# Optimization experiments

Hardware: AMD Instinct MI355X
Metric: run time of the kernel (lower is better)

## Reference

```python
import jax, jax.numpy as jnp
import numpy as np

B, S, H = 4, 2048, 2048          # batch, seq_len, hidden_size
NH, NKV, D = 8, 1, 256           # query heads, kv heads (MQA), head_dim
ROPE_THETA = 10000.0
SCALE = D ** -0.5


def setup_inputs() -> dict:
    key = jax.random.key(0)
    k1, k2, k3 = jax.random.split(key, 3)
    hidden_states = jax.random.normal(k1, (B, S, H), dtype=jnp.float32)
    w_qkv = jax.random.normal(k2, (H, (NH + 2 * NKV) * D), dtype=jnp.float32) * 0.02
    w_o = jax.random.normal(k3, (NH * D, H), dtype=jnp.float32) * 0.02
    positions = jnp.arange(S, dtype=jnp.int32)
    return {"hidden_states": hidden_states, "positions": positions,
            "w_qkv": w_qkv, "w_o": w_o}


def _apply_rope(x, positions):
    # x: [B, S, n_heads, D], neox style: rotate halves
    d2 = D // 2
    inv_freq = 1.0 / (ROPE_THETA ** (jnp.arange(0, d2, dtype=jnp.float32) * 2.0 / D))
    ang = positions.astype(jnp.float32)[:, None] * inv_freq[None, :]      # [S, d2]
    cos = jnp.cos(ang)[None, :, None, :]                                  # [1,S,1,d2]
    sin = jnp.sin(ang)[None, :, None, :]
    x1, x2 = x[..., :d2], x[..., d2:]
    return jnp.concatenate([x1 * cos - x2 * sin, x2 * cos + x1 * sin], axis=-1)


def reference(hidden_states, positions, w_qkv, w_o):
    # fused QKV projection
    qkv = jnp.einsum('bsh,hd->bsd', hidden_states, w_qkv)                 # [B,S,(NH+2NKV)*D]
    q_size, kv_size = NH * D, NKV * D
    q = qkv[..., :q_size].reshape(B, S, NH, D)
    k = qkv[..., q_size:q_size + kv_size].reshape(B, S, NKV, D)
    v = qkv[..., q_size + kv_size:].reshape(B, S, NKV, D)

    q = _apply_rope(q, positions)
    k = _apply_rope(k, positions)

    # expand KV heads for MQA/GQA
    rep = NH // NKV
    k = jnp.repeat(k, rep, axis=2)                                        # [B,S,NH,D]
    v = jnp.repeat(v, rep, axis=2)

    scores = jnp.einsum('bqhd,bkhd->bhqk', q, k) * SCALE                  # [B,NH,S,S]
    causal = jnp.tril(jnp.ones((S, S), dtype=bool))
    scores = jnp.where(causal[None, None], scores, jnp.finfo(scores.dtype).min)
    probs = jax.nn.softmax(scores, axis=-1)
    attn = jnp.einsum('bhqk,bkhd->bqhd', probs, v).reshape(B, S, NH * D)

    return jnp.einsum('bsd,dh->bsh', attn, w_o)                           # [B,S,H]
```

## Files before the change

### kernel.cpp

```cpp
#include <hip/hip_runtime.h>
#include <math.h>

constexpr int BATCH = 4;
constexpr int SEQ   = 2048;
constexpr int HID   = 2048;
constexpr int NHEAD = 8;
constexpr int HD    = 256;
constexpr int QKVN  = (NHEAD + 2) * HD;
constexpr float SCL = 0.0625f;

typedef __bf16 bf16_t;
typedef __bf16 bf16x8 __attribute__((ext_vector_type(8)));
typedef float  f32x4  __attribute__((ext_vector_type(4)));

__device__ __forceinline__ f32x4 zero4() {
  f32x4 z; z[0] = 0.f; z[1] = 0.f; z[2] = 0.f; z[3] = 0.f; return z;
}

__device__ __forceinline__ f32x4 mfma16(bf16x8 a, bf16x8 b, f32x4 c) {
  return __builtin_amdgcn_mfma_f32_16x16x32_bf16(a, b, c, 0, 0, 0);
}

__device__ __forceinline__ void gl2lds16(const void* g, void* lds) {
  typedef __attribute__((address_space(1))) void* gp_t;
  typedef __attribute__((address_space(3))) void* lp_t;
  __builtin_amdgcn_global_load_lds((gp_t)(size_t)g,
                                   (lp_t)(unsigned int)(size_t)lds, 16, 0, 0);
}

__device__ __forceinline__ float rmax16(float v) {
#pragma unroll
  for (int o = 1; o < 16; o <<= 1) v = fmaxf(v, __shfl_xor(v, o));
  return v;
}
__device__ __forceinline__ float rsum16(float v) {
#pragma unroll
  for (int o = 1; o < 16; o <<= 1) v += __shfl_xor(v, o);
  return v;
}

__global__ __launch_bounds__(256)
void cvt_bf16_kernel(const float* __restrict__ in, bf16_t* __restrict__ out) {
  const int i = blockIdx.x * 256 + threadIdx.x;
  const float4 a = ((const float4*)in)[i * 2];
  const float4 b = ((const float4*)in)[i * 2 + 1];
  bf16x8 o;
  o[0] = (bf16_t)a.x; o[1] = (bf16_t)a.y; o[2] = (bf16_t)a.z; o[3] = (bf16_t)a.w;
  o[4] = (bf16_t)b.x; o[5] = (bf16_t)b.y; o[6] = (bf16_t)b.z; o[7] = (bf16_t)b.w;
  ((bf16x8*)out)[i] = o;
}

__global__ __launch_bounds__(256)
void transw_kernel(const float* __restrict__ w, bf16_t* __restrict__ wT, int K, int N) {
  __shared__ __align__(16) bf16_t tile[64][72];
  const int n0 = blockIdx.x * 64, k0 = blockIdx.y * 64;
  const int t = threadIdx.x, rr = t >> 3, c8 = (t & 7) * 8;
#pragma unroll
  for (int it = 0; it < 2; ++it) {
    const int r = rr + it * 32;
    const float4* p = (const float4*)(w + (size_t)(k0 + r) * N + n0 + c8);
    const float4 a = p[0], b = p[1];
    bf16x8 o;
    o[0] = (bf16_t)a.x; o[1] = (bf16_t)a.y; o[2] = (bf16_t)a.z; o[3] = (bf16_t)a.w;
    o[4] = (bf16_t)b.x; o[5] = (bf16_t)b.y; o[6] = (bf16_t)b.z; o[7] = (bf16_t)b.w;
    *(bf16x8*)&tile[r][c8] = o;
  }
  __syncthreads();
#pragma unroll
  for (int it = 0; it < 2; ++it) {
    const int rn = rr + it * 32;
    bf16x8 o;
#pragma unroll
    for (int j = 0; j < 8; ++j) o[j] = tile[c8 + j][rn];
    *(bf16x8*)&wT[(size_t)(n0 + rn) * K + k0 + c8] = o;
  }
}

template <typename TC>
__global__ __launch_bounds__(256)
void gemm_bt_kernel(const bf16_t* __restrict__ A, const bf16_t* __restrict__ BT,
                    TC* __restrict__ C, int M, int N, int K) {
  __shared__ __align__(16) bf16_t As[128 * 32];
  __shared__ __align__(16) bf16_t Bs[128 * 32];
  const int tid = threadIdx.x;
  const int lane = tid & 63, w = tid >> 6;
  const int quad = lane >> 4, l15 = lane & 15;
  const int bm = blockIdx.y * 128, bn = blockIdx.x * 128;
  const int wm = (w & 1) * 64, wn = (w >> 1) * 64;
  const int r0 = tid >> 2, c0 = tid & 3;

  f32x4 acc[4][4];
#pragma unroll
  for (int mt = 0; mt < 4; ++mt)
#pragma unroll
    for (int nt = 0; nt < 4; ++nt) acc[mt][nt] = zero4();

  for (int k0 = 0; k0 < K; k0 += 32) {
#pragma unroll
    for (int i = 0; i < 2; ++i) {
      const int r = r0 + i * 64;
      const int cg = (c0 ^ (r & 3)) << 3;
      gl2lds16(A + (size_t)(bm + r) * K + k0 + cg, &As[(i * 256 + w * 64) * 8]);
      gl2lds16(BT + (size_t)(bn + r) * K + k0 + cg, &Bs[(i * 256 + w * 64) * 8]);
    }
    __syncthreads();
    bf16x8 af[4], bf[4];
#pragma unroll
    for (int mt = 0; mt < 4; ++mt) {
      const int row = wm + mt * 16 + l15;
      af[mt] = *(const bf16x8*)&As[row * 32 + ((quad ^ (row & 3)) << 3)];
    }
#pragma unroll
    for (int nt = 0; nt < 4; ++nt) {
      const int row = wn + nt * 16 + l15;
      bf[nt] = *(const bf16x8*)&Bs[row * 32 + ((quad ^ (row & 3)) << 3)];
    }
#pragma unroll
    for (int mt = 0; mt < 4; ++mt)
#pragma unroll
      for (int nt = 0; nt < 4; ++nt)
        acc[mt][nt] = mfma16(af[mt], bf[nt], acc[mt][nt]);
    __syncthreads();
  }

#pragma unroll
  for (int mt = 0; mt < 4; ++mt)
#pragma unroll
    for (int nt = 0; nt < 4; ++nt)
#pragma unroll
      for (int r = 0; r < 4; ++r) {
        const int row = bm + wm + mt * 16 + quad * 4 + r;
        const int col = bn + wn + nt * 16 + l15;
        C[(size_t)row * N + col] = (TC)acc[mt][nt][r];
      }
}

__global__ __launch_bounds__(128)
void rope_table_kernel(const int* __restrict__ pos, float2* __restrict__ tab) {
  const int s = blockIdx.x, i = threadIdx.x;
  const float inv_freq = powf(10000.0f, -(float)i / 128.0f);
  const float ang = (float)pos[s] * inv_freq;
  float sn, cs;
  sincosf(ang, &sn, &cs);
  tab[s * 128 + i] = make_float2(cs, sn);
}

__global__ __launch_bounds__(256)
void rope_kernel(const float2* __restrict__ tab, bf16_t* __restrict__ qkv) {
  const int bs = blockIdx.x * 16 + (threadIdx.x >> 4);
  const int h  = blockIdx.y;
  const int i0 = (threadIdx.x & 15) * 8;
  const int s  = bs & (SEQ - 1);
  const size_t base = (size_t)bs * QKVN + (size_t)h * HD;
  bf16x8 a = *(const bf16x8*)&qkv[base + i0];
  bf16x8 b = *(const bf16x8*)&qkv[base + 128 + i0];
  bf16x8 oa, ob;
#pragma unroll
  for (int j = 0; j < 8; ++j) {
    const float2 t = tab[s * 128 + i0 + j];
    const float x1 = (float)a[j], x2 = (float)b[j];
    oa[j] = (bf16_t)(x1 * t.x - x2 * t.y);
    ob[j] = (bf16_t)(x2 * t.x + x1 * t.y);
  }
  *(bf16x8*)&qkv[base + i0]       = oa;
  *(bf16x8*)&qkv[base + 128 + i0] = ob;
}

__global__ __launch_bounds__(256)
void vtrans_kernel(const bf16_t* __restrict__ qkv, bf16_t* __restrict__ Vt) {
  __shared__ __align__(16) bf16_t tile[64][72];
  const int s0 = blockIdx.x * 64, d0 = blockIdx.y * 64, b = blockIdx.z;
  const int t = threadIdx.x, rr = t >> 3, c8 = (t & 7) * 8;
#pragma unroll
  for (int it = 0; it < 2; ++it) {
    const int r = rr + it * 32;
    *(bf16x8*)&tile[r][c8] =
        *(const bf16x8*)&qkv[(size_t)(b * SEQ + s0 + r) * QKVN + 2304 + d0 + c8];
  }
  __syncthreads();
#pragma unroll
  for (int it = 0; it < 2; ++it) {
    const int dd = rr + it * 32;
    bf16x8 o;
#pragma unroll
    for (int j = 0; j < 8; ++j) o[j] = tile[c8 + j][dd];
    *(bf16x8*)&Vt[(size_t)(b * HD + d0 + dd) * SEQ + s0 + c8] = o;
  }
}

__global__ __launch_bounds__(512)
void attn_kernel(const bf16_t* __restrict__ qkv, const bf16_t* __restrict__ Vt,
                 bf16_t* __restrict__ O) {
  __shared__ __align__(16) bf16_t Ks[2][64 * 256];
  __shared__ __align__(16) bf16_t Vts[2][256 * 64];
  __shared__ __align__(16) bf16_t Pl[8][16][72];

  const int tid = threadIdx.x, w = tid >> 6, lane = tid & 63;
  const int quad = lane >> 4, l15 = lane & 15;
  const int b = blockIdx.x >> 6;
  const int qtR = blockIdx.x & 63;
  const int h = w;

  const int krow_base = w * 2 + (lane >> 5);
  const int kcol = lane & 31;
  const int vrow_base = w * 8 + (lane >> 3);
  const int vcol = lane & 7;

  const bf16_t* kbase0 = qkv + (size_t)(b * SEQ) * QKVN + 2048;
  const bf16_t* vbase0 = Vt + (size_t)b * HD * SEQ;

  auto stage = [&](int kt, int buf) {
    const bf16_t* kbase = kbase0 + (size_t)(kt * 64) * QKVN;
#pragma unroll
    for (int i = 0; i < 4; ++i) {
      const int r = i * 16 + krow_base;
      gl2lds16(kbase + (size_t)r * QKVN + ((kcol ^ (r & 31)) << 3),
               &Ks[buf][(i * 512 + w * 64) * 8]);
    }
    const bf16_t* vbase = vbase0 + kt * 64;
#pragma unroll
    for (int i = 0; i < 4; ++i) {
      const int r = i * 64 + vrow_base;
      gl2lds16(vbase + (size_t)r * SEQ + ((vcol ^ (r & 7)) << 3),
               &Vts[buf][(i * 512 + w * 64) * 8]);
    }
  };

  for (int phase = 0; phase < 2; ++phase) {
    const int qt = phase ? (127 - qtR) : qtR;
    const int q0 = qt * 16;

    bf16x8 qf[8];
    const bf16_t* qp =
        qkv + (size_t)(b * SEQ + q0 + l15) * QKVN + (size_t)h * HD + quad * 8;
#pragma unroll
    for (int ks = 0; ks < 8; ++ks) qf[ks] = *(const bf16x8*)(qp + ks * 32);

    float mrun[4], lrun[4];
    f32x4 of[16];
#pragma unroll
    for (int r = 0; r < 4; ++r) { mrun[r] = -3e38f; lrun[r] = 0.f; }
#pragma unroll
    for (int dt = 0; dt < 16; ++dt) of[dt] = zero4();

    const int ntiles = q0 / 64 + 1;
    int cur = 0;
    stage(0, 0);
    __syncthreads();

    for (int kt = 0; kt < ntiles; ++kt) {
      if (kt + 1 < ntiles) stage(kt + 1, cur ^ 1);

      const bf16_t* ksb = Ks[cur];
      const bf16_t* vsb = Vts[cur];

      f32x4 sf[4];
#pragma unroll
      for (int nt = 0; nt < 4; ++nt) {
        f32x4 acc = zero4();
        const int row = nt * 16 + l15;
#pragma unroll
        for (int ks = 0; ks < 8; ++ks) {
          const int j = ks * 4 + quad;
          const bf16x8 kf = *(const bf16x8*)&ksb[row * 256 + ((j ^ (row & 31)) << 3)];
          acc = mfma16(qf[ks], kf, acc);
        }
        sf[nt] = acc;
      }

      const bool lastTile = (kt == ntiles - 1);
      float mx[4];
#pragma unroll
      for (int r = 0; r < 4; ++r) {
        const int qg = q0 + quad * 4 + r;
        float v = -3e38f;
#pragma unroll
        for (int nt = 0; nt < 4; ++nt) {
          float s = sf[nt][r] * SCL;
          if (lastTile) {
            const int kg = kt * 64 + nt * 16 + l15;
            if (kg > qg) s = -3e38f;
          }
          sf[nt][r] = s;
          v = fmaxf(v, s);
        }
        mx[r] = rmax16(v);
      }

      float g = 0.f;
#pragma unroll
      for (int r = 0; r < 4; ++r) g = fmaxf(g, mx[r] - mrun[r]);
      const bool resc = !__all(g <= 8.0f);
      f32x4 av;
      if (resc) {
#pragma unroll
        for (int r = 0; r < 4; ++r) {
          const float mn = fmaxf(mrun[r], mx[r]);
          av[r] = __expf(mrun[r] - mn);
          mrun[r] = mn;
          lrun[r] *= av[r];
        }
      }

#pragma unroll
      for (int r = 0; r < 4; ++r) {
        float sum = 0.f;
#pragma unroll
        for (int nt = 0; nt < 4; ++nt) {
          const float pv = __expf(sf[nt][r] - mrun[r]);
          Pl[w][quad * 4 + r][nt * 16 + l15] = (bf16_t)pv;
          sum += pv;
        }
        lrun[r] += rsum16(sum);
      }
      if (resc) {
#pragma unroll
        for (int dt = 0; dt < 16; ++dt) of[dt] *= av;
      }
      __asm__ volatile("s_waitcnt lgkmcnt(0)" ::: "memory");

      bf16x8 pa[2];
#pragma unroll
      for (int k2 = 0; k2 < 2; ++k2)
        pa[k2] = *(const bf16x8*)&Pl[w][l15][k2 * 32 + quad * 8];
#pragma unroll
      for (int dt = 0; dt < 16; ++dt) {
        const int row = dt * 16 + l15;
#pragma unroll
        for (int k2 = 0; k2 < 2; ++k2) {
          const int j = k2 * 4 + quad;
          const bf16x8 vf = *(const bf16x8*)&vsb[row * 64 + ((j ^ (row & 7)) << 3)];
          of[dt] = mfma16(pa[k2], vf, of[dt]);
        }
      }

      __syncthreads();
      cur ^= 1;
    }

    f32x4 iv;
#pragma unroll
    for (int r = 0; r < 4; ++r) iv[r] = 1.0f / lrun[r];
#pragma unroll
    for (int dt = 0; dt < 16; ++dt) {
      const f32x4 o = of[dt] * iv;
#pragma unroll
      for (int r = 0; r < 4; ++r)
        O[(size_t)(b * SEQ + q0 + quad * 4 + r) * HID + (size_t)h * HD + dt * 16 + l15] =
            (bf16_t)o[r];
    }
  }
}

extern "C" void kernel_launch(void* const* d_in, const int* in_sizes, int n_in,
                              void* d_out, int out_size, void* d_ws, size_t ws_size,
                              hipStream_t stream) {
  const float* hidden  = (const float*)d_in[0];
  const int* positions = (const int*)d_in[1];
  const float* w_qkv   = (const float*)d_in[2];
  const float* w_o     = (const float*)d_in[3];
  float* out           = (float*)d_out;

  char* ws = (char*)d_ws;
  bf16_t* hiddenB = (bf16_t*)ws; ws += (size_t)8192 * 2048 * 2;
  bf16_t* wqkvT   = (bf16_t*)ws; ws += (size_t)2560 * 2048 * 2;
  bf16_t* woT     = (bf16_t*)ws; ws += (size_t)2048 * 2048 * 2;
  bf16_t* qkvB    = (bf16_t*)ws; ws += (size_t)8192 * 2560 * 2;
  bf16_t* VtB     = (bf16_t*)ws; ws += (size_t)4 * 256 * 2048 * 2;
  bf16_t* attnB   = (bf16_t*)ws;

  float2* ropeTab = (float2*)attnB;

  cvt_bf16_kernel<<<8192, 256, 0, stream>>>(hidden, hiddenB);
  transw_kernel<<<dim3(QKVN / 64, HID / 64), 256, 0, stream>>>(w_qkv, wqkvT, HID, QKVN);
  transw_kernel<<<dim3(HID / 64, HID / 64), 256, 0, stream>>>(w_o, woT, HID, HID);
  rope_table_kernel<<<SEQ, 128, 0, stream>>>(positions, ropeTab);

  gemm_bt_kernel<bf16_t><<<dim3(QKVN / 128, 64), 256, 0, stream>>>
      (hiddenB, wqkvT, qkvB, 8192, QKVN, HID);

  rope_kernel<<<dim3(BATCH * SEQ / 16, 9), 256, 0, stream>>>(ropeTab, qkvB);
  vtrans_kernel<<<dim3(SEQ / 64, HD / 64, BATCH), 256, 0, stream>>>(qkvB, VtB);

  attn_kernel<<<256, 512, 0, stream>>>(qkvB, VtB, attnB);

  gemm_bt_kernel<float><<<dim3(HID / 128, 64), 256, 0, stream>>>
      (attnB, woT, out, 8192, HID, HID);
}
```

Measured before the change: 510.0 us.

## Restructure attention to 32-row query tiles with 4-head blocks; swizzle GEMM block order

The attention kernel now uses 256-thread blocks of 4 heads, each wave processing two 16-row query subtiles that share every K/V fragment read from LDS. Double buffering is dropped so two blocks can fit per CU, and the P scratch buffer gets an XOR swizzle to avoid bank conflicts. The GEMM remaps block indices with an XCD-aware swizzle so neighbouring tiles land on the same L2. Without double buffering, the global loads are no longer overlapped with compute inside a block, and holding two accumulator sets raises register pressure.

```diff
diff --git a/kernel.cpp b/kernel.cpp
--- a/kernel.cpp
+++ b/kernel.cpp
@@ -85,7 +85,13 @@
   const int tid = threadIdx.x;
   const int lane = tid & 63, w = tid >> 6;
   const int quad = lane >> 4, l15 = lane & 15;
-  const int bm = blockIdx.y * 128, bn = blockIdx.x * 128;
+
+  const int nwg = gridDim.x * gridDim.y;
+  const int flat = blockIdx.y * gridDim.x + blockIdx.x;
+  const int cpx = nwg >> 3;
+  const int swz = (flat & 7) * cpx + (flat >> 3);
+  const int bm = (swz / gridDim.x) * 128, bn = (swz % gridDim.x) * 128;
+
   const int wm = (w & 1) * 64, wn = (w >> 1) * 64;
   const int r0 = tid >> 2, c0 = tid & 3;
 
@@ -188,18 +194,23 @@
   }
 }
 
-__global__ __launch_bounds__(512)
+__global__ __launch_bounds__(256, 2)
 void attn_kernel(const bf16_t* __restrict__ qkv, const bf16_t* __restrict__ Vt,
                  bf16_t* __restrict__ O) {
-  __shared__ __align__(16) bf16_t Ks[2][64 * 256];
-  __shared__ __align__(16) bf16_t Vts[2][256 * 64];
-  __shared__ __align__(16) bf16_t Pl[8][16][72];
+  __shared__ __align__(16) bf16_t Ks[64 * 256];
+  __shared__ __align__(16) bf16_t Vts[256 * 64];
+  __shared__ __align__(16) bf16_t Pl[4][32][64];
 
   const int tid = threadIdx.x, w = tid >> 6, lane = tid & 63;
   const int quad = lane >> 4, l15 = lane & 15;
-  const int b = blockIdx.x >> 6;
-  const int qtR = blockIdx.x & 63;
-  const int h = w;
+  const int bid = blockIdx.x;
+  const int j = bid & 255;
+  const int b = j >> 6;
+  const int hg = bid >> 8;
+  const int qg = hg ? (63 - (j & 63)) : (j & 63);
+  const int h = hg * 4 + w;
+  const int q0 = qg * 32;
+  const int ntiles = (q0 + 31) / 64 + 1;
 
   const int krow_base = w * 2 + (lane >> 5);
   const int kcol = lane & 31;
@@ -209,145 +220,154 @@
   const bf16_t* kbase0 = qkv + (size_t)(b * SEQ) * QKVN + 2048;
   const bf16_t* vbase0 = Vt + (size_t)b * HD * SEQ;
 
-  auto stage = [&](int kt, int buf) {
+  bf16x8 qf[2][8];
+#pragma unroll
+  for (int sub = 0; sub < 2; ++sub) {
+    const bf16_t* qp = qkv + (size_t)(b * SEQ + q0 + sub * 16 + l15) * QKVN +
+                       (size_t)h * HD + quad * 8;
+#pragma unroll
+    for (int ks = 0; ks < 8; ++ks) qf[sub][ks] = *(const bf16x8*)(qp + ks * 32);
+  }
+
+  float mrun[2][4], lrun[2][4];
+  f32x4 of[2][16];
+#pragma unroll
+  for (int sub = 0; sub < 2; ++sub) {
+#pragma unroll
+    for (int r = 0; r < 4; ++r) { mrun[sub][r] = -3e38f; lrun[sub][r] = 0.f; }
+#pragma unroll
+    for (int dt = 0; dt < 16; ++dt) of[sub][dt] = zero4();
+  }
+
+  for (int kt = 0; kt < ntiles; ++kt) {
     const bf16_t* kbase = kbase0 + (size_t)(kt * 64) * QKVN;
 #pragma unroll
-    for (int i = 0; i < 4; ++i) {
-      const int r = i * 16 + krow_base;
+    for (int i = 0; i < 8; ++i) {
+      const int r = i * 8 + krow_base;
       gl2lds16(kbase + (size_t)r * QKVN + ((kcol ^ (r & 31)) << 3),
-               &Ks[buf][(i * 512 + w * 64) * 8]);
+               &Ks[(i * 256 + w * 64) * 8]);
     }
     const bf16_t* vbase = vbase0 + kt * 64;
 #pragma unroll
-    for (int i = 0; i < 4; ++i) {
-      const int r = i * 64 + vrow_base;
+    for (int i = 0; i < 8; ++i) {
+      const int r = i * 32 + vrow_base;
       gl2lds16(vbase + (size_t)r * SEQ + ((vcol ^ (r & 7)) << 3),
-               &Vts[buf][(i * 512 + w * 64) * 8]);
-    }
-  };
-
-  for (int phase = 0; phase < 2; ++phase) {
-    const int qt = phase ? (127 - qtR) : qtR;
-    const int q0 = qt * 16;
-
-    bf16x8 qf[8];
-    const bf16_t* qp =
-        qkv + (size_t)(b * SEQ + q0 + l15) * QKVN + (size_t)h * HD + quad * 8;
-#pragma unroll
-    for (int ks = 0; ks < 8; ++ks) qf[ks] = *(const bf16x8*)(qp + ks * 32);
-
-    float mrun[4], lrun[4];
-    f32x4 of[16];
-#pragma unroll
-    for (int r = 0; r < 4; ++r) { mrun[r] = -3e38f; lrun[r] = 0.f; }
-#pragma unroll
-    for (int dt = 0; dt < 16; ++dt) of[dt] = zero4();
-
-    const int ntiles = q0 / 64 + 1;
-    int cur = 0;
-    stage(0, 0);
+               &Vts[(i * 256 + w * 64) * 8]);
+    }
     __syncthreads();
 
-    for (int kt = 0; kt < ntiles; ++kt) {
-      if (kt + 1 < ntiles) stage(kt + 1, cur ^ 1);
-
-      const bf16_t* ksb = Ks[cur];
-      const bf16_t* vsb = Vts[cur];
-
-      f32x4 sf[4];
-#pragma unroll
-      for (int nt = 0; nt < 4; ++nt) {
-        f32x4 acc = zero4();
-        const int row = nt * 16 + l15;
-#pragma unroll
-        for (int ks = 0; ks < 8; ++ks) {
-          const int j = ks * 4 + quad;
-          const bf16x8 kf = *(const bf16x8*)&ksb[row * 256 + ((j ^ (row & 31)) << 3)];
-          acc = mfma16(qf[ks], kf, acc);
-        }
-        sf[nt] = acc;
+    f32x4 sf[2][4];
+#pragma unroll
+    for (int nt = 0; nt < 4; ++nt) {
+      f32x4 a0 = zero4(), a1 = zero4();
+      const int row = nt * 16 + l15;
+#pragma unroll
+      for (int ks = 0; ks < 8; ++ks) {
+        const bf16x8 kf =
+            *(const bf16x8*)&Ks[row * 256 + (((ks * 4 + quad) ^ (row & 31)) << 3)];
+        a0 = mfma16(qf[0][ks], kf, a0);
+        a1 = mfma16(qf[1][ks], kf, a1);
       }
-
-      const bool lastTile = (kt == ntiles - 1);
-      float mx[4];
+      sf[0][nt] = a0; sf[1][nt] = a1;
+    }
+
+    const bool lastTile = (kt == ntiles - 1);
+    float mx[2][4];
+#pragma unroll
+    for (int sub = 0; sub < 2; ++sub)
 #pragma unroll
       for (int r = 0; r < 4; ++r) {
-        const int qg = q0 + quad * 4 + r;
+        const int qrow = q0 + sub * 16 + quad * 4 + r;
         float v = -3e38f;
 #pragma unroll
         for (int nt = 0; nt < 4; ++nt) {
-          float s = sf[nt][r] * SCL;
+          float s = sf[sub][nt][r] * SCL;
           if (lastTile) {
             const int kg = kt * 64 + nt * 16 + l15;
-            if (kg > qg) s = -3e38f;
+            if (kg > qrow) s = -3e38f;
           }
-          sf[nt][r] = s;
+          sf[sub][nt][r] = s;
           v = fmaxf(v, s);
         }
-        mx[r] = rmax16(v);
+        mx[sub][r] = rmax16(v);
       }
 
-      float g = 0.f;
-#pragma unroll
-      for (int r = 0; r < 4; ++r) g = fmaxf(g, mx[r] - mrun[r]);
-      const bool resc = !__all(g <= 8.0f);
-      f32x4 av;
-      if (resc) {
+    float g = 0.f;
+#pragma unroll
+    for (int sub = 0; sub < 2; ++sub)
+#pragma unroll
+      for (int r = 0; r < 4; ++r) g = fmaxf(g, mx[sub][r] - mrun[sub][r]);
+    const bool resc = !__all(g <= 8.0f);
+    f32x4 av[2];
+    if (resc) {
+#pragma unroll
+      for (int sub = 0; sub < 2; ++sub)
 #pragma unroll
         for (int r = 0; r < 4; ++r) {
-          const float mn = fmaxf(mrun[r], mx[r]);
-          av[r] = __expf(mrun[r] - mn);
-          mrun[r] = mn;
-          lrun[r] *= av[r];
+          const float mn = fmaxf(mrun[sub][r], mx[sub][r]);
+          av[sub][r] = __expf(mrun[sub][r] - mn);
+          mrun[sub][r] = mn;
+          lrun[sub][r] *= av[sub][r];
         }
-      }
-
+    }
+
+#pragma unroll
+    for (int sub = 0; sub < 2; ++sub)
 #pragma unroll
       for (int r = 0; r < 4; ++r) {
+        const int rowp = sub * 16 + quad * 4 + r;
         float sum = 0.f;
 #pragma unroll
         for (int nt = 0; nt < 4; ++nt) {
-          const float pv = __expf(sf[nt][r] - mrun[r]);
-          Pl[w][quad * 4 + r][nt * 16 + l15] = (bf16_t)pv;
+          const float pv = __expf(sf[sub][nt][r] - mrun[sub][r]);
+          Pl[w][rowp][(((nt * 2 + (l15 >> 3)) ^ (rowp & 7)) << 3) + (l15 & 7)] =
+              (bf16_t)pv;
           sum += pv;
         }
-        lrun[r] += rsum16(sum);
+        lrun[sub][r] += rsum16(sum);
       }
-      if (resc) {
-#pragma unroll
-        for (int dt = 0; dt < 16; ++dt) of[dt] *= av;
+    if (resc) {
+#pragma unroll
+      for (int sub = 0; sub < 2; ++sub)
+#pragma unroll
+        for (int dt = 0; dt < 16; ++dt) of[sub][dt] *= av[sub];
+    }
+    __asm__ volatile("s_waitcnt lgkmcnt(0)" ::: "memory");
+
+    bf16x8 pa[2][2];
+#pragma unroll
+    for (int sub = 0; sub < 2; ++sub)
+#pragma unroll
+      for (int k2 = 0; k2 < 2; ++k2)
+        pa[sub][k2] = *(const bf16x8*)
+            &Pl[w][sub * 16 + l15][(((k2 * 4 + quad) ^ (l15 & 7)) << 3)];
+#pragma unroll
+    for (int dt = 0; dt < 16; ++dt) {
+      const int row = dt * 16 + l15;
+#pragma unroll
+      for (int k2 = 0; k2 < 2; ++k2) {
+        const bf16x8 vf =
+            *(const bf16x8*)&Vts[row * 64 + (((k2 * 4 + quad) ^ (row & 7)) << 3)];
+        of[0][dt] = mfma16(pa[0][k2], vf, of[0][dt]);
+        of[1][dt] = mfma16(pa[1][k2], vf, of[1][dt]);
       }
-      __asm__ volatile("s_waitcnt lgkmcnt(0)" ::: "memory");
-
-      bf16x8 pa[2];
-#pragma unroll
-      for (int k2 = 0; k2 < 2; ++k2)
-        pa[k2] = *(const bf16x8*)&Pl[w][l15][k2 * 32 + quad * 8];
-#pragma unroll
-      for (int dt = 0; dt < 16; ++dt) {
-        const int row = dt * 16 + l15;
-#pragma unroll
-        for (int k2 = 0; k2 < 2; ++k2) {
-          const int j = k2 * 4 + quad;
-          const bf16x8 vf = *(const bf16x8*)&vsb[row * 64 + ((j ^ (row & 7)) << 3)];
-          of[dt] = mfma16(pa[k2], vf, of[dt]);
-        }
-      }
-
-      __syncthreads();
-      cur ^= 1;
-    }
-
+    }
+
+    __syncthreads();
+  }
+
+#pragma unroll
+  for (int sub = 0; sub < 2; ++sub) {
     f32x4 iv;
 #pragma unroll
-    for (int r = 0; r < 4; ++r) iv[r] = 1.0f / lrun[r];
+    for (int r = 0; r < 4; ++r) iv[r] = 1.0f / lrun[sub][r];
 #pragma unroll
     for (int dt = 0; dt < 16; ++dt) {
-      const f32x4 o = of[dt] * iv;
+      const f32x4 o = of[sub][dt] * iv;
 #pragma unroll
       for (int r = 0; r < 4; ++r)
-        O[(size_t)(b * SEQ + q0 + quad * 4 + r) * HID + (size_t)h * HD + dt * 16 + l15] =
-            (bf16_t)o[r];
+        O[(size_t)(b * SEQ + q0 + sub * 16 + quad * 4 + r) * HID +
+          (size_t)h * HD + dt * 16 + l15] = (bf16_t)o[r];
     }
   }
 }
@@ -382,7 +402,7 @@
   rope_kernel<<<dim3(BATCH * SEQ / 16, 9), 256, 0, stream>>>(ropeTab, qkvB);
   vtrans_kernel<<<dim3(SEQ / 64, HD / 64, BATCH), 256, 0, stream>>>(qkvB, VtB);
 
-  attn_kernel<<<256, 512, 0, stream>>>(qkvB, VtB, attnB);
+  attn_kernel<<<512, 256, 0, stream>>>(qkvB, VtB, attnB);
 
   gemm_bt_kernel<float><<<dim3(HID / 128, 64), 256, 0, stream>>>
       (attnB, woT, out, 8192, HID, HID);
```

After: 776.0 us. 1.52x slower.

## Replace GEMM with 256x256-tile, 512-thread double-buffered pipelined kernel

Applied to the files above, without the earlier changes.

Replaces the simple 128x128 single-buffered bf16 GEMM with a 256x256 tile kernel using 8 waves and a 64-wide K step. Global-to-LDS loads are double-buffered and interleaved with MFMA phases, using explicit waitcnt, barriers and setprio. The goal is to raise data reuse per tile and hide memory latency behind matrix math in both projection GEMMs. In exchange it needs 128KB of LDS, which limits occupancy, and launches fewer blocks (320 and 256), which risks poor CU fill on a 256-CU part.

```diff
diff --git a/kernel.cpp b/kernel.cpp
--- a/kernel.cpp
+++ b/kernel.cpp
@@ -76,63 +76,145 @@
   }
 }
 
+#define BAR()   __builtin_amdgcn_s_barrier()
+#define LGKM0() do { asm volatile("s_waitcnt lgkmcnt(0)" ::: "memory"); \
+                     __builtin_amdgcn_sched_barrier(0); } while (0)
+#define VMC(n)  asm volatile("s_waitcnt vmcnt(" #n ")" ::: "memory")
+
 template <typename TC>
-__global__ __launch_bounds__(256)
-void gemm_bt_kernel(const bf16_t* __restrict__ A, const bf16_t* __restrict__ BT,
+__global__ __launch_bounds__(512)
+void gemm256_kernel(const bf16_t* __restrict__ A, const bf16_t* __restrict__ BT,
                     TC* __restrict__ C, int M, int N, int K) {
-  __shared__ __align__(16) bf16_t As[128 * 32];
-  __shared__ __align__(16) bf16_t Bs[128 * 32];
+  __shared__ __align__(16) bf16_t As[2][2][128 * 64];
+  __shared__ __align__(16) bf16_t Bs[2][2][128 * 64];
+
   const int tid = threadIdx.x;
-  const int lane = tid & 63, w = tid >> 6;
+  const int w = tid >> 6, lane = tid & 63;
+  const int wr = w >> 2, wc = w & 3;
   const int quad = lane >> 4, l15 = lane & 15;
-  const int bm = blockIdx.y * 128, bn = blockIdx.x * 128;
-  const int wm = (w & 1) * 64, wn = (w >> 1) * 64;
-  const int r0 = tid >> 2, c0 = tid & 3;
-
-  f32x4 acc[4][4];
-#pragma unroll
-  for (int mt = 0; mt < 4; ++mt)
+  const int bm = blockIdx.y * 256, bn = blockIdx.x * 256;
+
+  const int srow = tid >> 3;
+  const int sc16 = (tid & 7) ^ (srow & 7);
+  const bf16_t* Asrc = A  + (size_t)(bm + srow) * K + sc16 * 8;
+  const bf16_t* Bsrc = BT + (size_t)(bn + srow) * K + sc16 * 8;
+
+#define STAGE_A(t, h) do {                                                  \
+    const bf16_t* _s = Asrc + (size_t)((h) * 128) * K + (t) * 64;           \
+    gl2lds16(_s,                 &As[(t) & 1][h][w * 512]);                 \
+    gl2lds16(_s + (size_t)64 * K, &As[(t) & 1][h][4096 + w * 512]);         \
+  } while (0)
+#define STAGE_B(t, h) do {                                                  \
+    const bf16_t* _s = Bsrc + (size_t)((h) * 128) * K + (t) * 64;           \
+    gl2lds16(_s,                 &Bs[(t) & 1][h][w * 512]);                 \
+    gl2lds16(_s + (size_t)64 * K, &Bs[(t) & 1][h][4096 + w * 512]);         \
+  } while (0)
+
+  const int c0  = ((quad ^ (l15 & 7)) << 3);
+  const int aro = l15 * 64;
+  const int bh  = wc >> 1;
+  const int bro = ((wc & 1) * 64 + l15) * 64;
+
+  f32x4 acc[8][4];
+#pragma unroll
+  for (int mt = 0; mt < 8; ++mt)
 #pragma unroll
     for (int nt = 0; nt < 4; ++nt) acc[mt][nt] = zero4();
 
-  for (int k0 = 0; k0 < K; k0 += 32) {
-#pragma unroll
-    for (int i = 0; i < 2; ++i) {
-      const int r = r0 + i * 64;
-      const int cg = (c0 ^ (r & 3)) << 3;
-      gl2lds16(A + (size_t)(bm + r) * K + k0 + cg, &As[(i * 256 + w * 64) * 8]);
-      gl2lds16(BT + (size_t)(bn + r) * K + k0 + cg, &Bs[(i * 256 + w * 64) * 8]);
-    }
-    __syncthreads();
-    bf16x8 af[4], bf[4];
-#pragma unroll
-    for (int mt = 0; mt < 4; ++mt) {
-      const int row = wm + mt * 16 + l15;
-      af[mt] = *(const bf16x8*)&As[row * 32 + ((quad ^ (row & 3)) << 3)];
-    }
-#pragma unroll
-    for (int nt = 0; nt < 4; ++nt) {
-      const int row = wn + nt * 16 + l15;
-      bf[nt] = *(const bf16x8*)&Bs[row * 32 + ((quad ^ (row & 3)) << 3)];
-    }
-#pragma unroll
-    for (int mt = 0; mt < 4; ++mt)
-#pragma unroll
-      for (int nt = 0; nt < 4; ++nt)
-        acc[mt][nt] = mfma16(af[mt], bf[nt], acc[mt][nt]);
-    __syncthreads();
-  }
-
-#pragma unroll
-  for (int mt = 0; mt < 4; ++mt)
+  bf16x8 bfr[4][2], a01[2][2], a2[6][2];
+
+#define LD_B(b) do { _Pragma("unroll")                                      \
+    for (int nt = 0; nt < 4; ++nt) {                                        \
+      bfr[nt][0] = *(const bf16x8*)&Bs[b][bh][bro + nt * 1024 + c0];        \
+      bfr[nt][1] = *(const bf16x8*)&Bs[b][bh][bro + nt * 1024 + (c0 ^ 32)]; \
+    } } while (0)
+#define LD_A01(b) do { _Pragma("unroll")                                    \
+    for (int mt = 0; mt < 2; ++mt) {                                        \
+      a01[mt][0] = *(const bf16x8*)&As[b][wr][aro + mt * 1024 + c0];        \
+      a01[mt][1] = *(const bf16x8*)&As[b][wr][aro + mt * 1024 + (c0 ^ 32)]; \
+    } } while (0)
+#define LD_A2(b) do { _Pragma("unroll")                                     \
+    for (int i = 0; i < 6; ++i) {                                           \
+      a2[i][0] = *(const bf16x8*)&As[b][wr][aro + (i + 2) * 1024 + c0];     \
+      a2[i][1] = *(const bf16x8*)&As[b][wr][aro + (i + 2) * 1024 + (c0^32)];\
+    } } while (0)
+#define MFMA8(A0, A1, mb) do {                                              \
+    __builtin_amdgcn_s_setprio(1);                                          \
+    _Pragma("unroll")                                                       \
+    for (int nt = 0; nt < 4; ++nt) {                                        \
+      acc[(mb)][nt]     = mfma16((A0)[0], bfr[nt][0], acc[(mb)][nt]);       \
+      acc[(mb)][nt]     = mfma16((A0)[1], bfr[nt][1], acc[(mb)][nt]);       \
+      acc[(mb)+1][nt]   = mfma16((A1)[0], bfr[nt][0], acc[(mb)+1][nt]);     \
+      acc[(mb)+1][nt]   = mfma16((A1)[1], bfr[nt][1], acc[(mb)+1][nt]);     \
+    }                                                                       \
+    __builtin_amdgcn_s_setprio(0);                                          \
+  } while (0)
+
+  const int NITER = K >> 7;
+
+  STAGE_A(0, 0); STAGE_A(0, 1); STAGE_B(0, 0); STAGE_B(0, 1);
+  STAGE_A(1, 0); STAGE_A(1, 1);
+  VMC(4);
+  BAR();
+
+  for (int u = 0; u < NITER; ++u) {
+    const bool last = (u == NITER - 1);
+    const int t1 = 2 * u + 1, t2 = 2 * u + 2, t3 = 2 * u + 3;
+
+    LD_B(0); LD_A01(0);
+    STAGE_B(t1, 0);
+    BAR(); LGKM0();
+    MFMA8(a01[0], a01[1], 0);
+    BAR();
+    LD_A2(0);
+    STAGE_B(t1, 1);
+    BAR(); LGKM0();
+    MFMA8(a2[0], a2[1], 2);
+    BAR();
+    if (!last) STAGE_A(t2, 0);
+    BAR();
+    MFMA8(a2[2], a2[3], 4);
+    BAR();
+    if (!last) { STAGE_A(t2, 1); VMC(4); } else { VMC(0); }
+    BAR();
+    MFMA8(a2[4], a2[5], 6);
+    BAR();
+    LD_B(1); LD_A01(1);
+    if (!last) STAGE_B(t2, 0);
+    BAR(); LGKM0();
+    MFMA8(a01[0], a01[1], 0);
+    BAR();
+    LD_A2(1);
+    if (!last) STAGE_B(t2, 1);
+    BAR(); LGKM0();
+    MFMA8(a2[0], a2[1], 2);
+    BAR();
+    if (!last) STAGE_A(t3, 0);
+    BAR();
+    MFMA8(a2[2], a2[3], 4);
+    BAR();
+    if (!last) { STAGE_A(t3, 1); VMC(4); }
+    BAR();
+    MFMA8(a2[4], a2[5], 6);
+    BAR();
+  }
+
+#pragma unroll
+  for (int mt = 0; mt < 8; ++mt)
 #pragma unroll
     for (int nt = 0; nt < 4; ++nt)
 #pragma unroll
       for (int r = 0; r < 4; ++r) {
-        const int row = bm + wm + mt * 16 + quad * 4 + r;
-        const int col = bn + wn + nt * 16 + l15;
+        const int row = bm + wr * 128 + mt * 16 + quad * 4 + r;
+        const int col = bn + wc * 64 + nt * 16 + l15;
         C[(size_t)row * N + col] = (TC)acc[mt][nt][r];
       }
+#undef STAGE_A
+#undef STAGE_B
+#undef LD_B
+#undef LD_A01
+#undef LD_A2
+#undef MFMA8
 }
 
 __global__ __launch_bounds__(128)
@@ -376,7 +458,7 @@
   transw_kernel<<<dim3(HID / 64, HID / 64), 256, 0, stream>>>(w_o, woT, HID, HID);
   rope_table_kernel<<<SEQ, 128, 0, stream>>>(positions, ropeTab);
 
-  gemm_bt_kernel<bf16_t><<<dim3(QKVN / 128, 64), 256, 0, stream>>>
+  gemm256_kernel<bf16_t><<<dim3(QKVN / 256, 8192 / 256), 512, 0, stream>>>
       (hiddenB, wqkvT, qkvB, 8192, QKVN, HID);
 
   rope_kernel<<<dim3(BATCH * SEQ / 16, 9), 256, 0, stream>>>(ropeTab, qkvB);
@@ -384,6 +466,6 @@
 
   attn_kernel<<<256, 512, 0, stream>>>(qkvB, VtB, attnB);
 
-  gemm_bt_kernel<float><<<dim3(HID / 128, 64), 256, 0, stream>>>
+  gemm256_kernel<float><<<dim3(HID / 256, 8192 / 256), 512, 0, stream>>>
       (attnB, woT, out, 8192, HID, HID);
 }
```

New measurement: 474.2 us. -7.0%, faster.
